# Kernel optimization log

Hardware: AMD Instinct MI355X
Metric: run time of the kernel (lower is better)

The kernel has to match this reference:

```python
import jax, jax.numpy as jnp
import numpy as np

ENCODED_DIM = 64
NUM_ENCODED = 512
BETA = 0.25


def setup_inputs() -> dict:
    key = jax.random.key(0)
    k1, k2 = jax.random.split(key)
    inputs = jax.random.normal(k1, (32, 64, 64, ENCODED_DIM), dtype=jnp.float32)
    # tf.random_uniform_initializer default: U[-0.05, 0.05]
    codebook = jax.random.uniform(k2, (ENCODED_DIM, NUM_ENCODED), dtype=jnp.float32,
                                  minval=-0.05, maxval=0.05)
    return {"inputs": inputs, "codebook": codebook}


def reference(inputs, codebook):
    original_shape = inputs.shape
    flat = inputs.reshape(-1, ENCODED_DIM)  # [N, D]
    # Squared Euclidean distances to each codebook column: [N, K]
    norms = (jnp.sum(flat ** 2, axis=1, keepdims=True)
             + jnp.sum(codebook ** 2, axis=0)
             - 2.0 * flat @ codebook)
    idx = jnp.argmin(norms, axis=1)  # [N]
    # one_hot @ codebook.T is exactly a row-gather of codebook.T
    quantized = jnp.take(codebook.T, idx, axis=0).reshape(original_shape)
    quantized_loss = jnp.mean((quantized - jax.lax.stop_gradient(inputs)) ** 2)
    commitment_loss = jnp.mean((jax.lax.stop_gradient(quantized) - inputs) ** 2)
    loss = BETA * commitment_loss + quantized_loss
    out = inputs + jax.lax.stop_gradient(quantized - inputs)
    return out, loss
```

## Files before the change

### kernel.cpp

```cpp
#include <hip/hip_runtime.h>
#include <math.h>

#define D 64
#define K 512
#define ROWS 131072
#define NELEM (ROWS * D)
#define TGAP 64.0f
#define FLAGBIT (1 << 30)
#define RPB 128
#define NBLK (ROWS / RPB)

typedef _Float16 half8 __attribute__((ext_vector_type(8)));
typedef float floatx4 __attribute__((ext_vector_type(4)));


__global__ __launch_bounds__(512) void vq_setup(const float* __restrict__ cb,
                                                _Float16* __restrict__ gH,
                                                _Float16* __restrict__ gL,
                                                float* __restrict__ Bn,
                                                unsigned long long* __restrict__ zws) {
    int idx = blockIdx.x * 512 + threadIdx.x;
    int k = idx >> 9, n = idx & 511;
    float c = cb[idx];
    float t = c * 4096.0f;
    _Float16 ch = (_Float16)t;
    float r = t - (float)ch;
    _Float16 cl = (_Float16)(r * 4096.0f);
    int off = (((n >> 4) * 2 + (k >> 5)) * 64 + ((k >> 3) & 3) * 16 + (n & 15)) * 8 + (k & 7);
    gH[off] = ch;
    gL[off] = cl;
    if (blockIdx.x == 1 && threadIdx.x < 4) zws[threadIdx.x] = 0ull;
    if (blockIdx.x == 0) {
#pragma clang fp contract(off)
        int j = threadIdx.x;
        float b = 0.f;
        for (int kk = 0; kk < D; ++kk) { float cc = cb[kk * K + j]; b = b + cc * cc; }
        Bn[j] = b * 0x1p20f;
    }
}

__global__ __launch_bounds__(256, 4) void vq_main(const float* __restrict__ x,
                                                  const float* __restrict__ cb,
                                                  const _Float16* __restrict__ gH,
                                                  const _Float16* __restrict__ gL,
                                                  const float* __restrict__ Bn,
                                                  float* __restrict__ out,
                                                  double* __restrict__ loss_acc,
                                                  unsigned int* __restrict__ ticket) {
    __shared__ float ldsB[K];
    __shared__ int rowinfo[4][32];
    __shared__ unsigned int flagbits[4];
    __shared__ float wavesum[4];

    const int tid = threadIdx.x;
    const int lane = tid & 63;
    const int w = tid >> 6;
    const int quad = lane >> 4;
    const int nn = lane & 15;

    ldsB[tid] = Bn[tid];
    ldsB[tid + 256] = Bn[tid + 256];
    if (tid < 4) flagbits[tid] = 0;

    const int rowBase = blockIdx.x * RPB + w * 32;

    half8 xh[2][2], xl[2][2];
    #pragma unroll
    for (int tt = 0; tt < 2; ++tt) {
        #pragma unroll
        for (int s = 0; s < 2; ++s) {
            const float* xp = x + (size_t)(rowBase + tt * 16 + nn) * D + s * 32 + quad * 8;
            float4 v0 = *(const float4*)xp;
            float4 v1 = *(const float4*)(xp + 4);
            float vv[8] = {v0.x, v0.y, v0.z, v0.w, v1.x, v1.y, v1.z, v1.w};
            #pragma unroll
            for (int j = 0; j < 8; ++j) {
                float t = vv[j] * -512.0f;
                _Float16 h = (_Float16)t;
                float r = t - (float)h;
                xh[tt][s][j] = h;
                xl[tt][s][j] = (_Float16)(r * 4096.0f);
            }
        }
    }
    __syncthreads();

    float m1[2][4], m2[2][4];
    int   i1[2][4];
    #pragma unroll
    for (int tt = 0; tt < 2; ++tt)
        #pragma unroll
        for (int r = 0; r < 4; ++r) { m1[tt][r] = INFINITY; m2[tt][r] = INFINITY; i1[tt][r] = 0; }

    const half8* bHp = (const half8*)gH;
    const half8* bLp = (const half8*)gL;

    #pragma unroll 2
    for (int t = 0; t < 32; ++t) {
        half8 bh0 = bHp[(t * 2 + 0) * 64 + lane];
        half8 bl0 = bLp[(t * 2 + 0) * 64 + lane];
        half8 bh1 = bHp[(t * 2 + 1) * 64 + lane];
        half8 bl1 = bLp[(t * 2 + 1) * 64 + lane];
        int col = t * 16 + nn;
        float Bj = ldsB[col];
        #pragma unroll
        for (int tt = 0; tt < 2; ++tt) {
            floatx4 a1 = {Bj, Bj, Bj, Bj};
            floatx4 a2 = {0.f, 0.f, 0.f, 0.f};
            a2 = __builtin_amdgcn_mfma_f32_16x16x32_f16(xl[tt][0], bh0, a2, 0, 0, 0);
            a2 = __builtin_amdgcn_mfma_f32_16x16x32_f16(xh[tt][0], bl0, a2, 0, 0, 0);
            a1 = __builtin_amdgcn_mfma_f32_16x16x32_f16(xh[tt][0], bh0, a1, 0, 0, 0);
            a2 = __builtin_amdgcn_mfma_f32_16x16x32_f16(xl[tt][1], bh1, a2, 0, 0, 0);
            a2 = __builtin_amdgcn_mfma_f32_16x16x32_f16(xh[tt][1], bl1, a2, 0, 0, 0);
            a1 = __builtin_amdgcn_mfma_f32_16x16x32_f16(xh[tt][1], bh1, a1, 0, 0, 0);
            #pragma unroll
            for (int r = 0; r < 4; ++r) {
                float g = fmaf(0x1p-12f, a2[r], a1[r]);
                float old1 = m1[tt][r];
                bool c1 = g < old1;
                m2[tt][r] = fminf(fmaxf(g, old1), m2[tt][r]);
                m1[tt][r] = c1 ? g : old1;
                i1[tt][r] = c1 ? col : i1[tt][r];
            }
        }
    }

    #pragma unroll
    for (int dlt = 1; dlt < 16; dlt <<= 1) {
        #pragma unroll
        for (int tt = 0; tt < 2; ++tt)
            #pragma unroll
            for (int r = 0; r < 4; ++r) {
                float om1 = __shfl_xor(m1[tt][r], dlt);
                int   oi1 = __shfl_xor(i1[tt][r], dlt);
                float om2 = __shfl_xor(m2[tt][r], dlt);
                bool ofirst = (om1 < m1[tt][r]) || (om1 == m1[tt][r] && oi1 < i1[tt][r]);
                float l1   = ofirst ? m1[tt][r] : om1;
                float cand = ofirst ? om2 : m2[tt][r];
                m1[tt][r] = ofirst ? om1 : m1[tt][r];
                i1[tt][r] = ofirst ? oi1 : i1[tt][r];
                m2[tt][r] = fminf(cand, l1);
            }
    }

    if (nn == 0) {
        #pragma unroll
        for (int tt = 0; tt < 2; ++tt)
            #pragma unroll
            for (int r = 0; r < 4; ++r) {
                int rl = tt * 16 + quad * 4 + r;
                bool flg = (m2[tt][r] - m1[tt][r]) < TGAP;
                rowinfo[w][rl] = i1[tt][r] | (flg ? FLAGBIT : 0);
                if (flg) atomicOr(&flagbits[w], 1u << rl);
            }
    }
    __syncthreads();

    float lsum = 0.f;
    #pragma unroll
    for (int tt = 0; tt < 2; ++tt) {
        #pragma unroll
        for (int p = 0; p < 4; ++p) {
            int rl = tt * 16 + p * 4 + quad;
            int info = rowinfo[w][rl];
            if (!(info & FLAGBIT)) {
                int j = info & 511;
                int kb = nn * 4;
                float q0 = cb[(kb + 0) * K + j];
                float q1 = cb[(kb + 1) * K + j];
                float q2 = cb[(kb + 2) * K + j];
                float q3 = cb[(kb + 3) * K + j];
                size_t row = (size_t)rowBase + rl;
                float4 xv = *(const float4*)(x + row * D + kb);
                float e0 = q0 - xv.x, e1 = q1 - xv.y, e2 = q2 - xv.z, e3 = q3 - xv.w;
                lsum += e0 * e0 + e1 * e1 + e2 * e2 + e3 * e3;
                *(float4*)(out + row * D + kb) = make_float4(q0, q1, q2, q3);
            }
        }
    }

    unsigned int fmask = flagbits[w];
    if (fmask) {
#pragma clang fp contract(off)
        float bn[8];
        #pragma unroll
        for (int m = 0; m < 8; ++m) bn[m] = 0.f;
        for (int k = 0; k < D; ++k) {
            const float* crow = cb + k * K + lane;
            #pragma unroll
            for (int m = 0; m < 8; ++m) {
                float c = crow[m * 64];
                bn[m] = bn[m] + c * c;
            }
        }
        while (fmask) {
            int b = __builtin_ctz(fmask);
            fmask &= fmask - 1;
            int row = rowBase + b;
            const float* xr = x + (size_t)row * D;
            float A0;
            {
                float rr[8];
                #pragma unroll
                for (int l = 0; l < 8; ++l) rr[l] = xr[l] * xr[l];
                #pragma unroll
                for (int m = 1; m < 8; ++m)
                    #pragma unroll
                    for (int l = 0; l < 8; ++l) {
                        float q = xr[8 * m + l] * xr[8 * m + l];
                        rr[l] = rr[l] + q;
                    }
                A0 = ((rr[0] + rr[1]) + (rr[2] + rr[3])) + ((rr[4] + rr[5]) + (rr[6] + rr[7]));
            }
            float a[8];
            #pragma unroll
            for (int m = 0; m < 8; ++m) a[m] = 0.f;
            for (int k = 0; k < D; ++k) {
                float xk = xr[k];
                const float* crow = cb + k * K + lane;
                #pragma unroll
                for (int m = 0; m < 8; ++m)
                    a[m] = fmaf(xk, crow[m * 64], a[m]);
            }
            float db = INFINITY; int jb = 0x7fffffff;
            #pragma unroll
            for (int m = 0; m < 8; ++m) {
                float s = A0 + bn[m];
                float t2 = 2.0f * a[m];
                float d = s - t2;
                int j = lane + (m << 6);
                if (d < db) { db = d; jb = j; }
            }
            for (int s = 1; s < 64; s <<= 1) {
                float od = __shfl_xor(db, s);
                int oj = __shfl_xor(jb, s);
                if ((od < db) || (od == db && oj < jb)) { db = od; jb = oj; }
            }
            float q = cb[lane * K + jb];
            out[(size_t)row * D + lane] = q;
            float e = q - xr[lane];
            lsum += e * e;
        }
    }

    #pragma unroll
    for (int off = 32; off > 0; off >>= 1) lsum += __shfl_down(lsum, off);
    if (lane == 0) wavesum[w] = lsum;
    __syncthreads();
    if (tid == 0) {
        double tot = (double)wavesum[0] + (double)wavesum[1]
                   + (double)wavesum[2] + (double)wavesum[3];
        atomicAdd(loss_acc, tot);
        __threadfence();
        unsigned int my = atomicAdd(ticket, 1u);
        if (my == (unsigned int)(gridDim.x - 1)) {
            double total = atomicAdd(loss_acc, 0.0);
            out[NELEM] = (float)(total * (1.25 / (double)NELEM));
        }
    }
}

extern "C" void kernel_launch(void* const* d_in, const int* in_sizes, int n_in,
                              void* d_out, int out_size, void* d_ws, size_t ws_size,
                              hipStream_t stream) {
    const float* x  = (const float*)d_in[0];
    const float* cb = (const float*)d_in[1];
    float* out = (float*)d_out;
    double* loss_acc     = (double*)d_ws;
    unsigned int* ticket = (unsigned int*)((char*)d_ws + 8);
    float* Bn        = (float*)((char*)d_ws + 4096);
    _Float16* gH     = (_Float16*)((char*)d_ws + 8192);
    _Float16* gL     = (_Float16*)((char*)d_ws + 73728);

    vq_setup<<<64, 512, 0, stream>>>(cb, gH, gL, Bn, (unsigned long long*)d_ws);
    vq_main<<<NBLK, 256, 0, stream>>>(x, cb, gH, gL, Bn, out, loss_acc, ticket);
}
```

Before: 206.7 us.

## Split codebook across wave pairs with 64-row tiles and LDS top-2 merge

Each wave now processes 64 rows against half of the codebook (256 entries) rather than 32 rows against all 512. This doubles the reuse of each loaded B fragment across row tiles and halves the global codebook traffic per wave. Per-row top-2 results from the two codebook halves are written to LDS and merged by 128 threads after an extra barrier. The setup kernel now iterates over the fragment-layout output so writes are coalesced, and the second-minimum update uses fmed3. The cost is higher register pressure (four row tiles of x fragments and accumulators) plus an extra synchronisation.

```diff
diff --git a/kernel.cpp b/kernel.cpp
--- a/kernel.cpp
+++ b/kernel.cpp
@@ -19,23 +19,24 @@
                                                 _Float16* __restrict__ gL,
                                                 float* __restrict__ Bn,
                                                 unsigned long long* __restrict__ zws) {
-    int idx = blockIdx.x * 512 + threadIdx.x;
-    int k = idx >> 9, n = idx & 511;
-    float c = cb[idx];
+    int off = blockIdx.x * 512 + threadIdx.x;
+    int j = off & 7;
+    int frag = off >> 3;
+    int n = ((frag >> 7) << 4) | (frag & 15);
+    int k = (((frag >> 6) & 1) << 5) | (((frag >> 4) & 3) << 3) | j;
+    float c = cb[k * K + n];
     float t = c * 4096.0f;
-    _Float16 ch = (_Float16)t;
-    float r = t - (float)ch;
-    _Float16 cl = (_Float16)(r * 4096.0f);
-    int off = (((n >> 4) * 2 + (k >> 5)) * 64 + ((k >> 3) & 3) * 16 + (n & 15)) * 8 + (k & 7);
-    gH[off] = ch;
-    gL[off] = cl;
+    _Float16 chh = (_Float16)t;
+    float r = t - (float)chh;
+    gH[off] = chh;
+    gL[off] = (_Float16)(r * 4096.0f);
     if (blockIdx.x == 1 && threadIdx.x < 4) zws[threadIdx.x] = 0ull;
     if (blockIdx.x == 0) {
 #pragma clang fp contract(off)
-        int j = threadIdx.x;
+        int jj = threadIdx.x;
         float b = 0.f;
-        for (int kk = 0; kk < D; ++kk) { float cc = cb[kk * K + j]; b = b + cc * cc; }
-        Bn[j] = b * 0x1p20f;
+        for (int kk = 0; kk < D; ++kk) { float cc = cb[kk * K + jj]; b = b + cc * cc; }
+        Bn[jj] = b * 0x1p20f;
     }
 }
 
@@ -48,13 +49,18 @@
                                                   double* __restrict__ loss_acc,
                                                   unsigned int* __restrict__ ticket) {
     __shared__ float ldsB[K];
-    __shared__ int rowinfo[4][32];
+    __shared__ float m1buf[4][64];
+    __shared__ float m2buf[4][64];
+    __shared__ int   i1buf[4][64];
+    __shared__ int   rowinfo[RPB];
     __shared__ unsigned int flagbits[4];
     __shared__ float wavesum[4];
 
     const int tid = threadIdx.x;
     const int lane = tid & 63;
     const int w = tid >> 6;
+    const int ch = w & 1;
+    const int rg = w >> 1;
     const int quad = lane >> 4;
     const int nn = lane & 15;
 
@@ -62,11 +68,12 @@
     ldsB[tid + 256] = Bn[tid + 256];
     if (tid < 4) flagbits[tid] = 0;
 
-    const int rowBase = blockIdx.x * RPB + w * 32;
-
-    half8 xh[2][2], xl[2][2];
-    #pragma unroll
-    for (int tt = 0; tt < 2; ++tt) {
+    const int blockBase = blockIdx.x * RPB;
+    const int rowBase = blockBase + rg * 64;
+
+    half8 xh[4][2], xl[4][2];
+    #pragma unroll
+    for (int tt = 0; tt < 4; ++tt) {
         #pragma unroll
         for (int s = 0; s < 2; ++s) {
             const float* xp = x + (size_t)(rowBase + tt * 16 + nn) * D + s * 32 + quad * 8;
@@ -74,21 +81,21 @@
             float4 v1 = *(const float4*)(xp + 4);
             float vv[8] = {v0.x, v0.y, v0.z, v0.w, v1.x, v1.y, v1.z, v1.w};
             #pragma unroll
-            for (int j = 0; j < 8; ++j) {
-                float t = vv[j] * -512.0f;
+            for (int jj = 0; jj < 8; ++jj) {
+                float t = vv[jj] * -512.0f;
                 _Float16 h = (_Float16)t;
                 float r = t - (float)h;
-                xh[tt][s][j] = h;
-                xl[tt][s][j] = (_Float16)(r * 4096.0f);
+                xh[tt][s][jj] = h;
+                xl[tt][s][jj] = (_Float16)(r * 4096.0f);
             }
         }
     }
     __syncthreads();
 
-    float m1[2][4], m2[2][4];
-    int   i1[2][4];
-    #pragma unroll
-    for (int tt = 0; tt < 2; ++tt)
+    float m1[4][4], m2[4][4];
+    int   i1[4][4];
+    #pragma unroll
+    for (int tt = 0; tt < 4; ++tt)
         #pragma unroll
         for (int r = 0; r < 4; ++r) { m1[tt][r] = INFINITY; m2[tt][r] = INFINITY; i1[tt][r] = 0; }
 
@@ -96,15 +103,16 @@
     const half8* bLp = (const half8*)gL;
 
     #pragma unroll 2
-    for (int t = 0; t < 32; ++t) {
-        half8 bh0 = bHp[(t * 2 + 0) * 64 + lane];
-        half8 bl0 = bLp[(t * 2 + 0) * 64 + lane];
-        half8 bh1 = bHp[(t * 2 + 1) * 64 + lane];
-        half8 bl1 = bLp[(t * 2 + 1) * 64 + lane];
-        int col = t * 16 + nn;
+    for (int t = 0; t < 16; ++t) {
+        int tg = ch * 16 + t;
+        half8 bh0 = bHp[(tg * 2 + 0) * 64 + lane];
+        half8 bl0 = bLp[(tg * 2 + 0) * 64 + lane];
+        half8 bh1 = bHp[(tg * 2 + 1) * 64 + lane];
+        half8 bl1 = bLp[(tg * 2 + 1) * 64 + lane];
+        int col = tg * 16 + nn;
         float Bj = ldsB[col];
         #pragma unroll
-        for (int tt = 0; tt < 2; ++tt) {
+        for (int tt = 0; tt < 4; ++tt) {
             floatx4 a1 = {Bj, Bj, Bj, Bj};
             floatx4 a2 = {0.f, 0.f, 0.f, 0.f};
             a2 = __builtin_amdgcn_mfma_f32_16x16x32_f16(xl[tt][0], bh0, a2, 0, 0, 0);
@@ -117,8 +125,8 @@
             for (int r = 0; r < 4; ++r) {
                 float g = fmaf(0x1p-12f, a2[r], a1[r]);
                 float old1 = m1[tt][r];
+                m2[tt][r] = __builtin_amdgcn_fmed3f(g, old1, m2[tt][r]);
                 bool c1 = g < old1;
-                m2[tt][r] = fminf(fmaxf(g, old1), m2[tt][r]);
                 m1[tt][r] = c1 ? g : old1;
                 i1[tt][r] = c1 ? col : i1[tt][r];
             }
@@ -128,7 +136,7 @@
     #pragma unroll
     for (int dlt = 1; dlt < 16; dlt <<= 1) {
         #pragma unroll
-        for (int tt = 0; tt < 2; ++tt)
+        for (int tt = 0; tt < 4; ++tt)
             #pragma unroll
             for (int r = 0; r < 4; ++r) {
                 float om1 = __shfl_xor(m1[tt][r], dlt);
@@ -145,37 +153,52 @@
 
     if (nn == 0) {
         #pragma unroll
-        for (int tt = 0; tt < 2; ++tt)
+        for (int tt = 0; tt < 4; ++tt)
             #pragma unroll
             for (int r = 0; r < 4; ++r) {
                 int rl = tt * 16 + quad * 4 + r;
-                bool flg = (m2[tt][r] - m1[tt][r]) < TGAP;
-                rowinfo[w][rl] = i1[tt][r] | (flg ? FLAGBIT : 0);
-                if (flg) atomicOr(&flagbits[w], 1u << rl);
+                m1buf[w][rl] = m1[tt][r];
+                m2buf[w][rl] = m2[tt][r];
+                i1buf[w][rl] = i1[tt][r];
             }
     }
     __syncthreads();
 
+    if (tid < RPB) {
+        int mrg = tid >> 6, mrl = tid & 63;
+        float a1v = m1buf[mrg * 2 + 0][mrl];
+        float a2v = m2buf[mrg * 2 + 0][mrl];
+        int   ai  = i1buf[mrg * 2 + 0][mrl];
+        float b1v = m1buf[mrg * 2 + 1][mrl];
+        float b2v = m2buf[mrg * 2 + 1][mrl];
+        int   bi  = i1buf[mrg * 2 + 1][mrl];
+        bool bf = b1v < a1v;
+        float f1 = bf ? b1v : a1v;
+        int   fi = bf ? bi : ai;
+        float f2 = fminf(fmaxf(a1v, b1v), bf ? b2v : a2v);
+        bool flg = (f2 - f1) < TGAP;
+        rowinfo[tid] = fi | (flg ? FLAGBIT : 0);
+        if (flg) atomicOr(&flagbits[tid >> 5], 1u << (tid & 31));
+    }
+    __syncthreads();
+
     float lsum = 0.f;
     #pragma unroll
-    for (int tt = 0; tt < 2; ++tt) {
-        #pragma unroll
-        for (int p = 0; p < 4; ++p) {
-            int rl = tt * 16 + p * 4 + quad;
-            int info = rowinfo[w][rl];
-            if (!(info & FLAGBIT)) {
-                int j = info & 511;
-                int kb = nn * 4;
-                float q0 = cb[(kb + 0) * K + j];
-                float q1 = cb[(kb + 1) * K + j];
-                float q2 = cb[(kb + 2) * K + j];
-                float q3 = cb[(kb + 3) * K + j];
-                size_t row = (size_t)rowBase + rl;
-                float4 xv = *(const float4*)(x + row * D + kb);
-                float e0 = q0 - xv.x, e1 = q1 - xv.y, e2 = q2 - xv.z, e3 = q3 - xv.w;
-                lsum += e0 * e0 + e1 * e1 + e2 * e2 + e3 * e3;
-                *(float4*)(out + row * D + kb) = make_float4(q0, q1, q2, q3);
-            }
+    for (int p = 0; p < 8; ++p) {
+        int rl = w * 32 + p * 4 + quad;
+        int info = rowinfo[rl];
+        if (!(info & FLAGBIT)) {
+            int j = info & 511;
+            int kb = nn * 4;
+            float q0 = cb[(kb + 0) * K + j];
+            float q1 = cb[(kb + 1) * K + j];
+            float q2 = cb[(kb + 2) * K + j];
+            float q3 = cb[(kb + 3) * K + j];
+            size_t row = (size_t)blockBase + rl;
+            float4 xv = *(const float4*)(x + row * D + kb);
+            float e0 = q0 - xv.x, e1 = q1 - xv.y, e2 = q2 - xv.z, e3 = q3 - xv.w;
+            lsum += e0 * e0 + e1 * e1 + e2 * e2 + e3 * e3;
+            *(float4*)(out + row * D + kb) = make_float4(q0, q1, q2, q3);
         }
     }
 
@@ -196,7 +219,7 @@
         while (fmask) {
             int b = __builtin_ctz(fmask);
             fmask &= fmask - 1;
-            int row = rowBase + b;
+            int row = blockBase + w * 32 + b;
             const float* xr = x + (size_t)row * D;
             float A0;
             {
```

Measured after the change: 280.4 us. 1.36x slower.

## Stage codebook fragments into LDS with double-buffered async global_load_lds

Applied to the files above, without the earlier changes.

Replaces per-wave direct global loads of the split-fp16 codebook fragments with a cooperative, double-buffered LDS staging pipeline using global_load_lds. Each wave fetches one quarter of every tile, and a block barrier separates iterations. The x scaling changes from -512 to 256, with the -2 factor and the codebook norm now applied in an fmaf after the MFMAs. The m2 update now uses fmed3. Launch bounds drop to 2 blocks per SU, which frees registers but adds a __syncthreads per iteration and may lower occupancy.

```diff
diff --git a/kernel.cpp b/kernel.cpp
--- a/kernel.cpp
+++ b/kernel.cpp
@@ -39,7 +39,7 @@
     }
 }
 
-__global__ __launch_bounds__(256, 4) void vq_main(const float* __restrict__ x,
+__global__ __launch_bounds__(256, 2) void vq_main(const float* __restrict__ x,
                                                   const float* __restrict__ cb,
                                                   const _Float16* __restrict__ gH,
                                                   const _Float16* __restrict__ gL,
@@ -48,6 +48,7 @@
                                                   double* __restrict__ loss_acc,
                                                   unsigned int* __restrict__ ticket) {
     __shared__ float ldsB[K];
+    __shared__ half8 bstage[2][2][4][64];
     __shared__ int rowinfo[4][32];
     __shared__ unsigned int flagbits[4];
     __shared__ float wavesum[4];
@@ -75,7 +76,7 @@
             float vv[8] = {v0.x, v0.y, v0.z, v0.w, v1.x, v1.y, v1.z, v1.w};
             #pragma unroll
             for (int j = 0; j < 8; ++j) {
-                float t = vv[j] * -512.0f;
+                float t = vv[j] * 256.0f;
                 _Float16 h = (_Float16)t;
                 float r = t - (float)h;
                 xh[tt][s][j] = h;
@@ -83,6 +84,18 @@
             }
         }
     }
+
+#define STAGE(buf, t_) do {                                                         \
+        const _Float16* gsrc = ((w & 1) ? gL : gH)                                  \
+                             + ((((t_) * 2 + (w >> 1)) * 64 + lane) * 8);           \
+        __builtin_amdgcn_global_load_lds(                                           \
+            (const __attribute__((address_space(1))) void*)gsrc,                    \
+            (__attribute__((address_space(3))) void*)&bstage[buf][(t_) & 1][w][0],  \
+            16, 0, 0);                                                              \
+    } while (0)
+
+    STAGE(0, 0);
+    STAGE(0, 1);
     __syncthreads();
 
     float m1[2][4], m2[2][4];
@@ -92,38 +105,43 @@
         #pragma unroll
         for (int r = 0; r < 4; ++r) { m1[tt][r] = INFINITY; m2[tt][r] = INFINITY; i1[tt][r] = 0; }
 
-    const half8* bHp = (const half8*)gH;
-    const half8* bLp = (const half8*)gL;
-
-    #pragma unroll 2
-    for (int t = 0; t < 32; ++t) {
-        half8 bh0 = bHp[(t * 2 + 0) * 64 + lane];
-        half8 bl0 = bLp[(t * 2 + 0) * 64 + lane];
-        half8 bh1 = bHp[(t * 2 + 1) * 64 + lane];
-        half8 bl1 = bLp[(t * 2 + 1) * 64 + lane];
-        int col = t * 16 + nn;
-        float Bj = ldsB[col];
-        #pragma unroll
-        for (int tt = 0; tt < 2; ++tt) {
-            floatx4 a1 = {Bj, Bj, Bj, Bj};
-            floatx4 a2 = {0.f, 0.f, 0.f, 0.f};
-            a2 = __builtin_amdgcn_mfma_f32_16x16x32_f16(xl[tt][0], bh0, a2, 0, 0, 0);
-            a2 = __builtin_amdgcn_mfma_f32_16x16x32_f16(xh[tt][0], bl0, a2, 0, 0, 0);
-            a1 = __builtin_amdgcn_mfma_f32_16x16x32_f16(xh[tt][0], bh0, a1, 0, 0, 0);
-            a2 = __builtin_amdgcn_mfma_f32_16x16x32_f16(xl[tt][1], bh1, a2, 0, 0, 0);
-            a2 = __builtin_amdgcn_mfma_f32_16x16x32_f16(xh[tt][1], bl1, a2, 0, 0, 0);
-            a1 = __builtin_amdgcn_mfma_f32_16x16x32_f16(xh[tt][1], bh1, a1, 0, 0, 0);
-            #pragma unroll
-            for (int r = 0; r < 4; ++r) {
-                float g = fmaf(0x1p-12f, a2[r], a1[r]);
-                float old1 = m1[tt][r];
-                bool c1 = g < old1;
-                m2[tt][r] = fminf(fmaxf(g, old1), m2[tt][r]);
-                m1[tt][r] = c1 ? g : old1;
-                i1[tt][r] = c1 ? col : i1[tt][r];
-            }
-        }
-    }
+    for (int p = 0; p < 16; ++p) {
+        const int cur = p & 1;
+        if (p < 15) { STAGE(cur ^ 1, 2 * p + 2); STAGE(cur ^ 1, 2 * p + 3); }
+        #pragma unroll
+        for (int h = 0; h < 2; ++h) {
+            const int t = 2 * p + h;
+            half8 bh0 = bstage[cur][h][0][lane];
+            half8 bl0 = bstage[cur][h][1][lane];
+            half8 bh1 = bstage[cur][h][2][lane];
+            half8 bl1 = bstage[cur][h][3][lane];
+            int col = t * 16 + nn;
+            float Bj = ldsB[col];
+            #pragma unroll
+            for (int tt = 0; tt < 2; ++tt) {
+                floatx4 a1 = {0.f, 0.f, 0.f, 0.f};
+                floatx4 a2 = {0.f, 0.f, 0.f, 0.f};
+                a2 = __builtin_amdgcn_mfma_f32_16x16x32_f16(xl[tt][0], bh0, a2, 0, 0, 0);
+                a2 = __builtin_amdgcn_mfma_f32_16x16x32_f16(xh[tt][0], bl0, a2, 0, 0, 0);
+                a1 = __builtin_amdgcn_mfma_f32_16x16x32_f16(xh[tt][0], bh0, a1, 0, 0, 0);
+                a2 = __builtin_amdgcn_mfma_f32_16x16x32_f16(xl[tt][1], bh1, a2, 0, 0, 0);
+                a2 = __builtin_amdgcn_mfma_f32_16x16x32_f16(xh[tt][1], bl1, a2, 0, 0, 0);
+                a1 = __builtin_amdgcn_mfma_f32_16x16x32_f16(xh[tt][1], bh1, a1, 0, 0, 0);
+                #pragma unroll
+                for (int r = 0; r < 4; ++r) {
+                    float macc = fmaf(0x1p-12f, a2[r], a1[r]);
+                    float g = fmaf(-2.0f, macc, Bj);
+                    float old1 = m1[tt][r];
+                    m2[tt][r] = __builtin_amdgcn_fmed3f(g, old1, m2[tt][r]);
+                    bool c1 = g < old1;
+                    m1[tt][r] = c1 ? g : old1;
+                    i1[tt][r] = c1 ? col : i1[tt][r];
+                }
+            }
+        }
+        __syncthreads();
+    }
+#undef STAGE
 
     #pragma unroll
     for (int dlt = 1; dlt < 16; dlt <<= 1) {
```

New measurement: 206.0 us. No clear change (-0.3%).
